# Optimization experiments

Hardware: AMD Instinct MI355X
Metric: run time of the kernel (lower is better)

## Reference

```python
import jax, jax.numpy as jnp
import numpy as np

C0, C1, ED, H, L, K = 128, 32, 64, 4, 2, 16
RADIUS = 16.0
EPS = 1e-6


def _ln(x, g, b):
    m = jnp.mean(x, -1, keepdims=True)
    v = jnp.var(x, -1, keepdims=True)
    return (x - m) * jax.lax.rsqrt(v + 1e-5) * g + b


def _gather_nodes(x, idx):
    # x [B,N,...], idx [B,N,K] -> [B,N,K,...]
    return jax.vmap(lambda xb, ib: xb[ib])(x, idx)


def _gather_pairs(e, idx):
    # e [B,N,N,ED], idx [B,N,K] -> [B,N,K,ED]  (batched_index_select on dim=2)
    return jax.vmap(lambda eb, ib: jnp.take_along_axis(eb, ib[..., None], axis=1))(e, idx)


def _fiber_norm(f0, f1, g0, b0, g1, b1):
    # deg-0: LayerNorm + gelu; deg-1: phase-preserving norm on channel magnitudes
    f0n = jax.nn.gelu(_ln(f0, g0, b0))
    n1 = jnp.linalg.norm(f1, axis=-1)                       # [B,N,C1]
    f1n = f1 / (n1 + EPS)[..., None] * jax.nn.gelu(_ln(n1, g1, b1))[..., None]
    return f0n, f1n


def _tfn_kv(f0j, f1j, y1, r, WA, WB):
    # Equivariant TFN edge kernel: paths 0->0(l=0), 1->0(l=1), 0->1(l=1),
    # 1->1(l=0), 1->1(l=1, cross), 1->1(l=2, traceless Y2) with radial gates r.
    r1, r2, r3, r4, r5, r6 = jnp.split(
        r, [C0, C0 + C1, 2 * C0 + C1, 2 * C0 + 2 * C1, 2 * C0 + 3 * C1], axis=-1)
    dot1 = jnp.einsum('bnkcm,bnkm->bnkc', f1j, y1)          # [B,N,K,C1]
    in0 = jnp.concatenate([r1 * f0j, r2 * dot1], -1)        # [B,N,K,C0+C1]
    k0 = jnp.einsum('oc,bnkc->bnko', WA, in0)               # [B,N,K,C0]
    p3 = (r3 * f0j)[..., None] * y1[..., None, :]           # [B,N,K,C0,3]
    p4 = r4[..., None] * f1j
    p5 = r5[..., None] * jnp.cross(f1j, y1[..., None, :])
    p6 = r6[..., None] * (y1[..., None, :] * dot1[..., None] - f1j / 3.0)
    in1 = jnp.concatenate([p3, p4, p5, p6], axis=-2)        # [B,N,K,C0+3*C1,3]
    k1 = jnp.einsum('oc,bnkcm->bnkom', WB, in1)             # [B,N,K,C1,3]
    return k0, k1


def reference(node_feats, pair_feats, coords, eln_g, eln_b, Wi0, Wi1,
              ln0_g, ln0_b, n1_g, n1_b, Wq0, Wq1, WrK, WrV, WkA, WkB, WvA, WvB,
              Wb, Wo0, Wo1, alpha_attn, lnf0_g, lnf0_b, nf1_g, nf1_b,
              Wf0a, Wf0b, Wf1a, Wf1b, alpha_ff, Wp0, Wp1):
    B, N = node_feats.shape[:2]
    Na, CA, Cc, Oo = [coords[..., i, :] for i in range(4)]          # each [B,N,3]
    f1_in = jnp.stack([Na, Cc, Oo], axis=-2) - CA[..., None, :]     # [B,N,3,3]
    # kNN graph on CA coords (exclude self), radius mask at 16A
    d2 = jnp.sum((CA[:, :, None] - CA[:, None, :]) ** 2, -1)        # [B,N,N]
    d2 = d2 + jnp.eye(N, dtype=d2.dtype) * 1e9
    nv, idx = jax.lax.top_k(-d2, K)                                 # idx [B,N,K]
    dist = jnp.sqrt(jnp.maximum(-nv, 0.0))
    mask = dist <= RADIUS
    rel_pos = _gather_nodes(CA, idx) - CA[:, :, None]               # [B,N,K,3]
    rel_b = jax.lax.stop_gradient(rel_pos)                          # basis on detached rel_pos
    y1 = rel_b / (jnp.linalg.norm(rel_b, axis=-1, keepdims=True) + EPS)
    edges = _ln(_gather_pairs(pair_feats, idx), eln_g, eln_b)       # [B,N,K,ED]
    # project in
    f0 = jnp.einsum('oc,bnc->bno', Wi0, node_feats)                 # [B,N,C0]
    f1 = jnp.einsum('oc,bncm->bnom', Wi1, f1_in)                    # [B,N,C1,3]
    dh0, dh1 = C0 // H, C1 // H
    scale = 1.0 / np.sqrt(dh0 + 3 * dh1)
    for l in range(L):
        # ---- attention block (prenorm -> TFN attention -> rezero residual)
        x0, x1 = _fiber_norm(f0, f1, ln0_g[l], ln0_b[l], n1_g[l], n1_b[l])
        q0 = jnp.einsum('oc,bnc->bno', Wq0[l], x0)
        q1 = jnp.einsum('oc,bncm->bnom', Wq1[l], x1)
        x0j = _gather_nodes(x0, idx)                                # [B,N,K,C0]
        x1j = _gather_nodes(x1, idx)                                # [B,N,K,C1,3]
        rk = jnp.einsum('re,bnke->bnkr', WrK[l], edges)
        rv = jnp.einsum('re,bnke->bnkr', WrV[l], edges)
        k0, k1 = _tfn_kv(x0j, x1j, y1, rk, WkA[l], WkB[l])
        v0, v1 = _tfn_kv(x0j, x1j, y1, rv, WvA[l], WvB[l])
        q0h = q0.reshape(B, N, H, dh0)
        q1h = q1.reshape(B, N, H, dh1, 3)
        k0h = k0.reshape(B, N, K, H, dh0)
        k1h = k1.reshape(B, N, K, H, dh1, 3)
        v0h = v0.reshape(B, N, K, H, dh0)
        v1h = v1.reshape(B, N, K, H, dh1, 3)
        logits = (jnp.einsum('bnhc,bnkhc->bnhk', q0h, k0h)
                  + jnp.einsum('bnhcm,bnkhcm->bnhk', q1h, k1h)) * scale
        logits = logits + jnp.einsum('he,bnke->bnhk', Wb[l], edges)
        logits = jnp.where(mask[:, :, None, :], logits, -1e9)
        attn = jax.nn.softmax(logits, axis=-1)
        o0 = jnp.einsum('bnhk,bnkhc->bnhc', attn, v0h).reshape(B, N, C0)
        o1 = jnp.einsum('bnhk,bnkhcm->bnhcm', attn, v1h).reshape(B, N, C1, 3)
        f0 = f0 + alpha_attn[l] * jnp.einsum('oc,bnc->bno', Wo0[l], o0)
        f1 = f1 + alpha_attn[l] * jnp.einsum('oc,bncm->bnom', Wo1[l], o1)
        # ---- fiber feedforward (prenorm -> FF -> rezero residual)
        x0, x1 = _fiber_norm(f0, f1, lnf0_g[l], lnf0_b[l], nf1_g[l], nf1_b[l])
        h0 = jnp.einsum('oh,bnh->bno', Wf0b[l],
                        jax.nn.gelu(jnp.einsum('hc,bnc->bnh', Wf0a[l], x0)))
        h1 = jnp.einsum('hc,bncm->bnhm', Wf1a[l], x1)
        nh = jnp.linalg.norm(h1, axis=-1)
        h1 = h1 * (jax.nn.gelu(nh) / (nh + EPS))[..., None]
        h1 = jnp.einsum('oh,bnhm->bnom', Wf1b[l], h1)
        f0 = f0 + alpha_ff[l] * h0
        f1 = f1 + alpha_ff[l] * h1
    # project out + _to_output
    node_out = jnp.einsum('oc,bnc->bno', Wp0, f0)                   # [B,N,128]
    coords_out = CA[:, :, None, :] + jnp.einsum('oc,bncm->bnom', Wp1, f1)  # [B,N,3,3]
    return node_out, coords_out


def setup_inputs() -> dict:
    key = jax.random.key(0)
    ks = iter(jax.random.split(key, 64))
    def rn(shape, scale=1.0):
        return (jax.random.normal(next(ks), shape) * scale).astype(jnp.float32)
    B, N = 1, 1024
    RC = 2 * C0 + 4 * C1
    ca = jnp.cumsum(rn((B, N, 3), 1.5), axis=1)          # protein-like chain
    coords = ca[:, :, None, :] + rn((B, N, 4, 3), 0.5)
    inp = dict(
        node_feats=rn((B, N, 128)),
        pair_feats=rn((B, N, N, ED)),
        coords=coords,
        eln_g=jnp.ones((ED,), jnp.float32), eln_b=jnp.zeros((ED,), jnp.float32),
        Wi0=rn((C0, 128), 128 ** -0.5), Wi1=rn((C1, 3), 3 ** -0.5),
        ln0_g=jnp.ones((L, C0), jnp.float32), ln0_b=jnp.zeros((L, C0), jnp.float32),
        n1_g=jnp.ones((L, C1), jnp.float32), n1_b=jnp.zeros((L, C1), jnp.float32),
        Wq0=rn((L, C0, C0), C0 ** -0.5), Wq1=rn((L, C1, C1), C1 ** -0.5),
        WrK=rn((L, RC, ED), ED ** -0.5), WrV=rn((L, RC, ED), ED ** -0.5),
        WkA=rn((L, C0, C0 + C1), (C0 + C1) ** -0.5),
        WkB=rn((L, C1, C0 + 3 * C1), (C0 + 3 * C1) ** -0.5),
        WvA=rn((L, C0, C0 + C1), (C0 + C1) ** -0.5),
        WvB=rn((L, C1, C0 + 3 * C1), (C0 + 3 * C1) ** -0.5),
        Wb=rn((L, H, ED), ED ** -0.5),
        Wo0=rn((L, C0, C0), C0 ** -0.5), Wo1=rn((L, C1, C1), C1 ** -0.5),
        alpha_attn=jnp.full((L,), 0.5, jnp.float32),
        lnf0_g=jnp.ones((L, C0), jnp.float32), lnf0_b=jnp.zeros((L, C0), jnp.float32),
        nf1_g=jnp.ones((L, C1), jnp.float32), nf1_b=jnp.zeros((L, C1), jnp.float32),
        Wf0a=rn((L, 4 * C0, C0), C0 ** -0.5), Wf0b=rn((L, C0, 4 * C0), (4 * C0) ** -0.5),
        Wf1a=rn((L, 4 * C1, C1), C1 ** -0.5), Wf1b=rn((L, C1, 4 * C1), (4 * C1) ** -0.5),
        alpha_ff=jnp.full((L,), 0.5, jnp.float32),
        Wp0=rn((128, C0), C0 ** -0.5), Wp1=rn((3, C1), C1 ** -0.5),
    )
    return inp
```

## Files before the change

### kernel.cpp

```cpp
#include <hip/hip_runtime.h>
#include <hip/hip_bf16.h>
#include <math.h>

static constexpr int NN  = 1024;
static constexpr int KK  = 16;
static constexpr int C0c = 128;
static constexpr int C1c = 32;
static constexpr int EDc = 64;
static constexpr int Lc  = 2;
static constexpr int ENUM = NN * KK;
static constexpr int PL   = NN * C1c;
static constexpr int X1HS = NN * 32;
#define SCALE_ATTN 0.13363062095621219f

typedef __attribute__((ext_vector_type(8))) short s8v;
typedef __attribute__((ext_vector_type(4))) float f4v;

__device__ __forceinline__ float wsum64(float v) {
    for (int o = 32; o > 0; o >>= 1) v += __shfl_xor(v, o);
    return v;
}
__device__ __forceinline__ float gsum16(float v) {
    for (int o = 8; o > 0; o >>= 1) v += __shfl_xor(v, o, 16);
    return v;
// ... 52 lines not shown
        const int wid = tid >> 6, lane = tid & 63;
        const int n = (bx - cvb) * 4 + wid;
        const float cx = ca[n * 3 + 0], cy = ca[n * 3 + 1], cz = ca[n * 3 + 2];
        float d[16];
#pragma unroll
        for (int s = 0; s < 16; ++s) {
            int i = s * 64 + lane;
            float dx = cx - ca[i * 3 + 0], dy = cy - ca[i * 3 + 1], dz = cz - ca[i * 3 + 2];
            float d2 = dx * dx + dy * dy + dz * dz;
            d[s] = (i == n) ? 1e9f : d2;
        }
        for (int t = 0; t < KK; ++t) {
            float best = 1e30f; int bi = 0;
#pragma unroll
            for (int s = 0; s < 16; ++s) {
                int i = s * 64 + lane;
                float v = d[s];
                if (v < best || (v == best && i < bi)) { best = v; bi = i; }
            }
#pragma unroll
            for (int o = 32; o > 0; o >>= 1) {
                float ov = __shfl_xor(best, o);
                int   oi = __shfl_xor(bi, o);
                if (ov < best || (ov == best && oi < bi)) { best = ov; bi = oi; }
            }
            const int j = bi;
            if (lane == 0) {
                idx[n * KK + t] = j;
                float dist = sqrtf(best);
                maskf[n * KK + t] = (dist <= 16.0f) ? 1.0f : 0.0f;
                float rx = ca[j * 3 + 0] - cx, ry = ca[j * 3 + 1] - cy, rz = ca[j * 3 + 2] - cz;
                float nrm = sqrtf(rx * rx + ry * ry + rz * rz) + 1e-6f;
                y1[(n * KK + t) * 3 + 0] = rx / nrm;
                y1[(n * KK + t) * 3 + 1] = ry / nrm;
                y1[(n * KK + t) * 3 + 2] = rz / nrm;
            }
            const int js = j >> 6, jl = j & 63;
#pragma unroll
            for (int s = 0; s < 16; ++s)
                if (s == js && jl == lane) d[s] = 2e30f;
        }
        return;
    }
    int g = (bx - cvb - 256) * 256 + tid;
    if (g >= NN * 32) return;
    int n = g >> 5, c = g & 31;
    float w0 = Wi1[c * 3 + 0], w1 = Wi1[c * 3 + 1], w2 = Wi1[c * 3 + 2];
#pragma unroll
    for (int m = 0; m < 3; ++m) {
        float cav = coords[(n * 4 + 1) * 3 + m];
        float a0 = coords[(n * 4 + 0) * 3 + m] - cav;
        float a1 = coords[(n * 4 + 2) * 3 + m] - cav;
        float a2 = coords[(n * 4 + 3) * 3 + m] - cav;
        f1p[m * PL + n * 32 + c] = w0 * a0 + w1 * a1 + w2 * a2;
    }
}

__global__ __launch_bounds__(256) void edge_f0_kernel(const float* __restrict__ pair,
                                                      const int* __restrict__ idx,
                                                      const float* __restrict__ g,
                                                      const float* __restrict__ b,
                                                      const float* __restrict__ Wb,
                                                      unsigned short* __restrict__ edges_h,
                                                      float* __restrict__ biasb,
                                                      const unsigned short* __restrict__ nf_h,
                                                      const unsigned short* __restrict__ Wi0_h,
                                                      float* __restrict__ f0) {
    const int t = threadIdx.x, wid = t >> 6, lane = t & 63;
    if (blockIdx.x < ENUM / 4) {
        const int e = blockIdx.x * 4 + wid;
        const int n = e >> 4;
        const int j = idx[e];
        float v = pair[((size_t)n * NN + j) * EDc + lane];
        float m = wsum64(v) * (1.0f / 64.0f);
        float d = v - m;
        float var = wsum64(d * d) * (1.0f / 64.0f);
        float nv = d * rsqrtf(var + 1e-5f) * g[lane] + b[lane];
        edges_h[e * EDc + lane] = f2bf(nv);
#pragma unroll
        for (int l = 0; l < 2; ++l)
#pragma unroll
            for (int h = 0; h < 4; ++h) {
                float tt = wsum64(nv * Wb[(l * 4 + h) * 64 + lane]);
                if (lane == 0) biasb[(size_t)l * ENUM * 4 + e * 4 + h] = tt;
            }
        return;
    }
    int rel = blockIdx.x - ENUM / 4;
    const int mt = rel & 7, ntc = rel >> 3;
    const int m0 = mt * 128 + wid * 32, n0 = ntc * 32;
    const int c16 = lane & 15, g8 = (lane >> 4) * 8, g4 = (lane >> 4) * 4;
    f4v acc[2][2];
#pragma unroll
    for (int a = 0; a < 2; ++a)
#pragma unroll
        for (int bq = 0; bq < 2; ++bq) acc[a][bq] = f4v{0.f, 0.f, 0.f, 0.f};
    const unsigned short* Ap = nf_h + (size_t)(m0 + c16) * 128 + g8;
    const unsigned short* Bp = Wi0_h + (size_t)(n0 + c16) * 128 + g8;
#pragma unroll
    for (int kc = 0; kc < 128; kc += 32) {
        s8v a0 = ld8(Ap + kc);
        s8v a1 = ld8(Ap + 16 * 128 + kc);
        s8v b0 = ld8(Bp + kc);
        s8v b1 = ld8(Bp + 16 * 128 + kc);
        acc[0][0] = mfma16(a0, b0, acc[0][0]);
        acc[0][1] = mfma16(a0, b1, acc[0][1]);
        acc[1][0] = mfma16(a1, b0, acc[1][0]);
        acc[1][1] = mfma16(a1, b1, acc[1][1]);
    }
#pragma unroll
    for (int fm = 0; fm < 2; ++fm)
#pragma unroll
        for (int r = 0; r < 4; ++r) {
            const int m = m0 + fm * 16 + g4 + r;
#pragma unroll
            for (int fn = 0; fn < 2; ++fn)
                f0[(size_t)m * 128 + n0 + fn * 16 + c16] = acc[fm][fn][r];
        }
}

__global__ __launch_bounds__(256) void fnorm1_kernel(const float* __restrict__ f0,
                                                     const float* __restrict__ f1p,
                                                     const float* __restrict__ g0,
                                                     const float* __restrict__ b0,
                                                     const float* __restrict__ g1,
                                                     const float* __restrict__ b1,
                                                     unsigned short* __restrict__ x0h,
                                                     unsigned short* __restrict__ x1h) {
    const int wid = threadIdx.x >> 6, lane = threadIdx.x & 63;
    const int n = blockIdx.x * 4 + wid;
    float va = f0[n * 128 + lane], vb = f0[n * 128 + lane + 64];
    float m = wsum64(va + vb) * (1.0f / 128.0f);
    float da = va - m, db = vb - m;
    float var = wsum64(da * da + db * db) * (1.0f / 128.0f);
    float rs = rsqrtf(var + 1e-5f);
    x0h[n * 128 + lane]      = f2bf(gelu_f(da * rs * g0[lane] + b0[lane]));
    x0h[n * 128 + lane + 64] = f2bf(gelu_f(db * rs * g0[lane + 64] + b0[lane + 64]));
    int c = lane & 31;
    float h0 = f1p[0 * PL + n * 32 + c];
    float h1 = f1p[1 * PL + n * 32 + c];
    float h2 = f1p[2 * PL + n * 32 + c];
    float n1 = sqrtf(h0 * h0 + h1 * h1 + h2 * h2);
    float ms = wsum64(n1) * (1.0f / 64.0f);
    float dd = n1 - ms;
    float vv = wsum64(dd * dd) * (1.0f / 64.0f);
    float sc = gelu_f(dd * rsqrtf(vv + 1e-5f) * g1[c] + b1[c]) / (n1 + 1e-6f);
    if (lane < 32) {
        x1h[0 * X1HS + n * 32 + c] = f2bf(h0 * sc);
        x1h[1 * X1HS + n * 32 + c] = f2bf(h1 * sc);
        x1h[2 * X1HS + n * 32 + c] = f2bf(h2 * sc);
    }
}

static constexpr int EKV_LDS = (64 * 168 + 64 * 136 + 3 * 64 * 104) * 2;

__global__ __launch_bounds__(256) void edge_kv_kernel(
    const unsigned short* __restrict__ edges_h,
    const unsigned short* __restrict__ WrK, const unsigned short* __restrict__ WrV,
    const unsigned short* __restrict__ WkA, const unsigned short* __restrict__ WvA,
    const unsigned short* __restrict__ WkB, const unsigned short* __restrict__ WvB,
    const unsigned short* __restrict__ x0h, const unsigned short* __restrict__ x1h,
    const int* __restrict__ idx, const float* __restrict__ y1,
    unsigned short* __restrict__ k0h, unsigned short* __restrict__ v0h,
    unsigned short* __restrict__ uKh, unsigned short* __restrict__ uVh,
    unsigned short* __restrict__ k1ph, unsigned short* __restrict__ v1ph,
    const unsigned short* __restrict__ Wq0l, const unsigned short* __restrict__ Wq1l,
    float* __restrict__ q0, float* __restrict__ q1p) {
    extern __shared__ unsigned short lsm[];
    const int t = threadIdx.x, w = t >> 6, l = t & 63;
    const int c16 = l & 15, g8 = (l >> 4) * 8, g4 = (l >> 4) * 4;
    const int bid = blockIdx.x;
    if (bid < 512) {
        unsigned short* in0L = lsm;
        unsigned short* inUL = lsm + 64 * 168;
        unsigned short* inWL = lsm + 64 * 168 + 64 * 136;
        const int s = bid >> 8, et = bid & 255, e0 = et * 64;
        const unsigned short* Wr = s ? WrV : WrK;
        const unsigned short* WA = s ? WvA : WkA;
        const unsigned short* WB = s ? WvB : WkB;
        unsigned short* K0o = s ? v0h : k0h;
        unsigned short* Uo  = s ? uVh : uKh;
        unsigned short* K1o = s ? v1ph : k1ph;
#pragma unroll 1
        for (int ti = w; ti < 24; ti += 4) {
            const int esub = ti & 1, rt = ti >> 1;
            const int e0w = e0 + esub * 32, r0 = rt * 32;
            f4v acc[2][2];
#pragma unroll
            for (int a = 0; a < 2; ++a)
#pragma unroll
                for (int bq = 0; bq < 2; ++bq) acc[a][bq] = f4v{0.f, 0.f, 0.f, 0.f};
#pragma unroll
            for (int kc = 0; kc < 64; kc += 32) {
                s8v a0 = ld8(edges_h + (size_t)(e0w + c16) * 64 + kc + g8);
                s8v a1 = ld8(edges_h + (size_t)(e0w + 16 + c16) * 64 + kc + g8);
                s8v b0 = ld8(Wr + (size_t)(r0 + c16) * 64 + kc + g8);
                s8v b1 = ld8(Wr + (size_t)(r0 + 16 + c16) * 64 + kc + g8);
                acc[0][0] = mfma16(a0, b0, acc[0][0]);
                acc[0][1] = mfma16(a0, b1, acc[0][1]);
                acc[1][0] = mfma16(a1, b0, acc[1][0]);
                acc[1][1] = mfma16(a1, b1, acc[1][1]);
            }
#pragma unroll
            for (int fm = 0; fm < 2; ++fm)
#pragma unroll
                for (int r = 0; r < 4; ++r) {
                    const int el = esub * 32 + fm * 16 + g4 + r;
                    const int e = e0 + el;
                    const int j = idx[e];
                    float ya = y1[e * 3 + 0], yb = y1[e * 3 + 1], yc = y1[e * 3 + 2];
#pragma unroll
                    for (int fn = 0; fn < 2; ++fn) {
                        const float av = acc[fm][fn][r];
                        const int col = r0 + fn * 16 + c16;
                        if (r0 < 128) {
                            in0L[el * 168 + col] = f2bf(av * bf2f(x0h[j * 128 + col]));
                        } else if (r0 < 160) {
                            int c = col - 128;
                            float d1 = bf2f(x1h[0 * X1HS + j * 32 + c]) * ya
                                     + bf2f(x1h[1 * X1HS + j * 32 + c]) * yb
                                     + bf2f(x1h[2 * X1HS + j * 32 + c]) * yc;
                            in0L[el * 168 + col] = f2bf(av * d1);
                        } else if (r0 < 288) {
                            int c = col - 160;
                            inUL[el * 136 + c] = f2bf(av * bf2f(x0h[j * 128 + c]));
                        } else {
                            int c = (r0 < 320) ? (col - 288) : (r0 < 352) ? (col - 320) : (col - 352);
                            float fx = bf2f(x1h[0 * X1HS + j * 32 + c]);
                            float fy = bf2f(x1h[1 * X1HS + j * 32 + c]);
                            float fz = bf2f(x1h[2 * X1HS + j * 32 + c]);
                            float w0, w1, w2; int off;
                            if (r0 < 320) {
                                off = 0; w0 = av * fx; w1 = av * fy; w2 = av * fz;
                            } else if (r0 < 352) {
                                off = 32;
                                w0 = av * (fy * yc - fz * yb);
                                w1 = av * (fz * ya - fx * yc);
                                w2 = av * (fx * yb - fy * ya);
                            } else {
                                off = 64;
                                float d1 = fx * ya + fy * yb + fz * yc;
                                w0 = av * (ya * d1 - fx * (1.0f / 3.0f));
                                w1 = av * (yb * d1 - fy * (1.0f / 3.0f));
                                w2 = av * (yc * d1 - fz * (1.0f / 3.0f));
                            }
                            inWL[0 * 64 * 104 + el * 104 + off + c] = f2bf(w0);
                            inWL[1 * 64 * 104 + el * 104 + off + c] = f2bf(w1);
                            inWL[2 * 64 * 104 + el * 104 + off + c] = f2bf(w2);
                        }
                    }
                }
        }
        __syncthreads();
#pragma unroll 1
        for (int ti = w; ti < 16; ti += 4) {
            const unsigned short* Ab; const unsigned short* Bb;
            unsigned short* Cb;
            int apit, K, ldb, ldcq, esub;
            if (ti < 8) {
                esub = ti & 1; int nt = ti >> 1;
                Ab = in0L; apit = 168; K = 160;
                Bb = WA + (size_t)(nt * 32) * 160; ldb = 160;
                Cb = K0o + (size_t)(e0 + esub * 32) * 128 + nt * 32; ldcq = 128;
            } else if (ti < 10) {
                esub = ti - 8;
                Ab = inUL; apit = 136; K = 128; Bb = WB; ldb = 224;
                Cb = Uo + (size_t)(e0 + esub * 32) * 32; ldcq = 32;
            } else {
                int id = ti - 10; int m = id >> 1; esub = id & 1;
                Ab = inWL + m * 64 * 104; apit = 104; K = 96;
                Bb = WB + 128; ldb = 224;
                Cb = K1o + ((size_t)m * ENUM + e0 + esub * 32) * 32; ldcq = 32;
            }
            const int m0l = esub * 32;
            f4v acc[2][2];
#pragma unroll
            for (int a = 0; a < 2; ++a)
#pragma unroll
                for (int bq = 0; bq < 2; ++bq) acc[a][bq] = f4v{0.f, 0.f, 0.f, 0.f};
            for (int kc = 0; kc < K; kc += 32) {
                s8v a0 = *(const s8v*)&Ab[(m0l + c16) * apit + kc + g8];
                s8v a1 = *(const s8v*)&Ab[(m0l + 16 + c16) * apit + kc + g8];
                s8v b0 = ld8(Bb + (size_t)c16 * ldb + kc + g8);
                s8v b1 = ld8(Bb + (size_t)(16 + c16) * ldb + kc + g8);
                acc[0][0] = mfma16(a0, b0, acc[0][0]);
                acc[0][1] = mfma16(a0, b1, acc[0][1]);
                acc[1][0] = mfma16(a1, b0, acc[1][0]);
                acc[1][1] = mfma16(a1, b1, acc[1][1]);
            }
#pragma unroll
            for (int fm = 0; fm < 2; ++fm)
#pragma unroll
                for (int r = 0; r < 4; ++r) {
                    const int lr = fm * 16 + g4 + r;
#pragma unroll
                    for (int fn = 0; fn < 2; ++fn)
                        Cb[(size_t)lr * ldcq + fn * 16 + c16] = f2bf(acc[fm][fn][r]);
                }
        }
        return;
    }
    const int rel = bid - 512;
    const unsigned short* A; const unsigned short* B;
    float* C; int K, lda2, ldb2, ldc2, m0, n0;
    if (rel < 32) {
        int mt = rel & 7, nt = rel >> 3;
        A = x0h; B = Wq0l; C = q0;
        K = 128; lda2 = 128; ldb2 = 128; ldc2 = 128;
        m0 = mt * 128 + w * 32; n0 = nt * 32;
    } else {
        int k = rel - 32; int pl = k >> 3; int mt = k & 7;
        A = x1h + (size_t)pl * X1HS; B = Wq1l; C = q1p + (size_t)pl * PL;
        K = 32; lda2 = 32; ldb2 = 32; ldc2 = 32;
        m0 = mt * 128 + w * 32; n0 = 0;
    }
    f4v acc[2][2];
#pragma unroll
    for (int a = 0; a < 2; ++a)
#pragma unroll
        for (int bq = 0; bq < 2; ++bq) acc[a][bq] = f4v{0.f, 0.f, 0.f, 0.f};
    const unsigned short* Ap = A + (size_t)(m0 + c16) * lda2 + g8;
    const unsigned short* Bp = B + (size_t)(n0 + c16) * ldb2 + g8;
    for (int kc = 0; kc < K; kc += 32) {
        s8v a0 = ld8(Ap + kc);
        s8v a1 = ld8(Ap + 16 * lda2 + kc);
        s8v b0 = ld8(Bp + kc);
        s8v b1 = ld8(Bp + 16 * ldb2 + kc);
        acc[0][0] = mfma16(a0, b0, acc[0][0]);
        acc[0][1] = mfma16(a0, b1, acc[0][1]);
        acc[1][0] = mfma16(a1, b0, acc[1][0]);
        acc[1][1] = mfma16(a1, b1, acc[1][1]);
    }
#pragma unroll
    for (int fm = 0; fm < 2; ++fm)
#pragma unroll
        for (int r = 0; r < 4; ++r) {
            const int m = m0 + fm * 16 + g4 + r;
#pragma unroll
            for (int fn = 0; fn < 2; ++fn)
                C[(size_t)m * ldc2 + n0 + fn * 16 + c16] = acc[fm][fn][r];
        }
}

__global__ __launch_bounds__(256) void attn_core(const float* __restrict__ q0,
                                                 const float* __restrict__ q1p,
                                                 const unsigned short* __restrict__ k0h,
                                                 const unsigned short* __restrict__ k1ph,
                                                 const unsigned short* __restrict__ v0h,
                                                 const unsigned short* __restrict__ v1ph,
                                                 const unsigned short* __restrict__ uKh,
                                                 const unsigned short* __restrict__ uVh,
                                                 const float* __restrict__ biasb,
                                                 const float* __restrict__ maskf,
                                                 const float* __restrict__ y1,
                                                 unsigned short* __restrict__ o0h,
                                                 unsigned short* __restrict__ o1h) {
    __shared__ float q0s[4][128];
    __shared__ float q1s[4][96];
    __shared__ float attns[4][64];
    const int wid = threadIdx.x >> 6, lane = threadIdx.x & 63;
    const int n = blockIdx.x * 4 + wid;
    q0s[wid][lane]      = q0[n * 128 + lane];
    q0s[wid][lane + 64] = q0[n * 128 + lane + 64];
    if (lane < 32) {
#pragma unroll
        for (int m = 0; m < 3; ++m) q1s[wid][m * 32 + lane] = q1p[m * PL + n * 32 + lane];
    }
    __syncthreads();
    {
        const int h = lane >> 4, k = lane & 15;
        const int e = n * KK + k;
        float acc = 0.f;
        const unsigned short* kr = k0h + (size_t)e * 128 + h * 32;
#pragma unroll
        for (int c8 = 0; c8 < 4; ++c8) {
            s8v kv = ld8(kr + c8 * 8);
#pragma unroll
            for (int j = 0; j < 8; ++j)
                acc += q0s[wid][h * 32 + c8 * 8 + j] * bf2f((unsigned short)kv[j]);
        }
        s8v uv = ld8(uKh + (size_t)e * 32 + h * 8);
#pragma unroll
        for (int m = 0; m < 3; ++m) {
            float yv = y1[e * 3 + m];
            s8v k1v = ld8(k1ph + ((size_t)m * ENUM + e) * 32 + h * 8);
#pragma unroll
            for (int c = 0; c < 8; ++c)
                acc += q1s[wid][m * 32 + h * 8 + c] *
                       (bf2f((unsigned short)k1v[c]) + bf2f((unsigned short)uv[c]) * yv);
        }
        acc = acc * SCALE_ATTN + biasb[e * 4 + h];
        if (maskf[e] == 0.0f) acc = -1e9f;
        float mx = gmax16(acc);
        float ex = expf(acc - mx);
        float sm = gsum16(ex);
        attns[wid][lane] = ex / sm;
    }
    __syncthreads();
    const int g = lane & 15, kq = lane >> 4;
    {
        float o[8] = {};
        const float* aw = &attns[wid][(g >> 2) * 16];
#pragma unroll
        for (int kk2 = 0; kk2 < 4; ++kk2) {
            int kk = kq * 4 + kk2;
            float a = aw[kk];
            s8v v = ld8(v0h + (size_t)(n * KK + kk) * 128 + g * 8);
#pragma unroll
            for (int j = 0; j < 8; ++j) o[j] += a * bf2f((unsigned short)v[j]);
        }
#pragma unroll
        for (int j = 0; j < 8; ++j) {
            o[j] += __shfl_xor(o[j], 16);
            o[j] += __shfl_xor(o[j], 32);
        }
        if (kq == 0) {
            s8v r;
#pragma unroll
            for (int j = 0; j < 8; ++j) r[j] = (short)f2bf(o[j]);
            *(s8v*)&o0h[(size_t)n * 128 + g * 8] = r;
        }
    }
    {
        float o[8] = {};
        const int plane = g >> 2, cg = g & 3;
        if (g < 12) {
            const float* aw = &attns[wid][cg * 16];
#pragma unroll
            for (int kk2 = 0; kk2 < 4; ++kk2) {
                int kk = kq * 4 + kk2;
                int e2 = n * KK + kk;
                float a = aw[kk];
                float yv = y1[e2 * 3 + plane];
                s8v v = ld8(v1ph + ((size_t)plane * ENUM + e2) * 32 + cg * 8);
                s8v u = ld8(uVh + (size_t)e2 * 32 + cg * 8);
#pragma unroll
                for (int j = 0; j < 8; ++j)
                    o[j] += a * (bf2f((unsigned short)v[j]) + bf2f((unsigned short)u[j]) * yv);
            }
        }
#pragma unroll
        for (int j = 0; j < 8; ++j) {
            o[j] += __shfl_xor(o[j], 16);
            o[j] += __shfl_xor(o[j], 32);
        }
        if (kq == 0 && g < 12) {
            s8v r;
#pragma unroll
            for (int j = 0; j < 8; ++j) r[j] = (short)f2bf(o[j]);
            *(s8v*)&o1h[((size_t)plane * NN + n) * 32 + cg * 8] = r;
        }
    }
}

template <int MODE>
__global__ __launch_bounds__(512) void fused_post(
    const unsigned short* __restrict__ o0h, const unsigned short* __restrict__ o1h,
    float* __restrict__ f0, float* __restrict__ f1p,
    const unsigned short* __restrict__ Wo0h, const unsigned short* __restrict__ Wo1h,
    const unsigned short* __restrict__ Wf0ah, const unsigned short* __restrict__ Wf0bh,
    const unsigned short* __restrict__ Wf1ah, const unsigned short* __restrict__ Wf1bh,
    const float* __restrict__ alA, const float* __restrict__ alF,
    const float* __restrict__ lnf0_g, const float* __restrict__ lnf0_b,
    const float* __restrict__ nf1_g, const float* __restrict__ nf1_b,
    const float* __restrict__ ln0n_g, const float* __restrict__ ln0n_b,
    const float* __restrict__ n1n_g, const float* __restrict__ n1n_b,
    unsigned short* __restrict__ x0h, unsigned short* __restrict__ x1h,
    const unsigned short* __restrict__ Wp0h, const float* __restrict__ Wp1,
    const float* __restrict__ coords, float* __restrict__ out) {
    __shared__ float f0s[16][132];
    __shared__ float f1s[3][16][36];
    __shared__ unsigned short x0s[16][136];
    __shared__ float x1s[3][16][36];
    __shared__ unsigned short hs[16][520];
    __shared__ unsigned short h1b[3][16][136];
    const int t = threadIdx.x, w = t >> 6, l = t & 63;
    const int c16 = l & 15, g8 = (l >> 4) * 8, g4 = (l >> 4) * 4;
    const int n0 = blockIdx.x * 16;
    const float aA = alA[0], aF = alF[0];

// ... 151 lines not shown
            }
            float s = gsum16(n1v[0] + n1v[1]);
            float mn = s * (1.0f / 32.0f);
            float d0 = n1v[0] - mn, d1 = n1v[1] - mn;
            float vv = gsum16(d0 * d0 + d1 * d1);
            float rs = rsqrtf(vv * (1.0f / 32.0f) + 1e-5f);
#pragma unroll
            for (int q = 0; q < 2; ++q) {
                int c = sub + q * 16;
                float sc = gelu_f((n1v[q] - mn) * rs * n1n_g[c] + n1n_b[c]) / (n1v[q] + 1e-6f);
                x1h[(size_t)0 * X1HS + (n0 + node) * 32 + c] = f2bf(p[q][0] * sc);
                x1h[(size_t)1 * X1HS + (n0 + node) * 32 + c] = f2bf(p[q][1] * sc);
                x1h[(size_t)2 * X1HS + (n0 + node) * 32 + c] = f2bf(p[q][2] * sc);
            }
        }
    } else {
#pragma unroll
        for (int it = 0; it < 4; ++it) {
            int g = t + it * 512;
            int row = g >> 7, col = g & 127;
            x0s[row][col] = f2bf(f0s[row][col]);
        }
        __syncthreads();
        f4v acc = f4v{0.f, 0.f, 0.f, 0.f};
#pragma unroll
        for (int kc = 0; kc < 128; kc += 32) {
            s8v a = *(const s8v*)&x0s[c16][kc + g8];
            s8v b = ld8(Wp0h + (size_t)(w * 16 + c16) * 128 + g8 + kc);
            acc = mfma16(a, b, acc);
        }
        int colg = w * 16 + c16;
#pragma unroll
        for (int r = 0; r < 4; ++r)
            out[(size_t)(n0 + g4 + r) * 128 + colg] = acc[r];
        if (t < 144) {
            int node = t / 9, rr = t % 9, o = rr / 3, m = rr % 3;
            float a = coords[((size_t)(n0 + node) * 4 + 1) * 3 + m];
            for (int c = 0; c < 32; ++c) a += Wp1[o * 32 + c] * f1s[m][node][c];
            out[NN * 128 + ((size_t)(n0 + node) * 3 + o) * 3 + m] = a;
        }
    }
}

extern "C" void kernel_launch(void* const* d_in, const int* in_sizes, int n_in,
                              void* d_out, int out_size, void* d_ws, size_t ws_size,
                              hipStream_t stream) {
    (void)in_sizes; (void)n_in; (void)out_size; (void)ws_size;
    const float* node_feats = (const float*)d_in[0];
    const float* pair       = (const float*)d_in[1];
    const float* coords     = (const float*)d_in[2];
    const float* eln_g      = (const float*)d_in[3];
    const float* eln_b      = (const float*)d_in[4];
    const float* Wi0        = (const float*)d_in[5];
    const float* Wi1        = (const float*)d_in[6];
    const float* ln0_g      = (const float*)d_in[7];
    const float* ln0_b      = (const float*)d_in[8];
    const float* n1_g       = (const float*)d_in[9];
    const float* n1_b       = (const float*)d_in[10];
    const float* Wq0        = (const float*)d_in[11];
    const float* Wq1        = (const float*)d_in[12];
    const float* WrK        = (const float*)d_in[13];
    const float* WrV        = (const float*)d_in[14];
    const float* WkA        = (const float*)d_in[15];
    const float* WkB        = (const float*)d_in[16];
    const float* WvA        = (const float*)d_in[17];
    const float* WvB        = (const float*)d_in[18];
    const float* Wb         = (const float*)d_in[19];
    const float* Wo0        = (const float*)d_in[20];
    const float* Wo1        = (const float*)d_in[21];
    const float* alpha_attn = (const float*)d_in[22];
    const float* lnf0_g     = (const float*)d_in[23];
    const float* lnf0_b     = (const float*)d_in[24];
    const float* nf1_g      = (const float*)d_in[25];
    const float* nf1_b      = (const float*)d_in[26];
    const float* Wf0a       = (const float*)d_in[27];
    const float* Wf0b       = (const float*)d_in[28];
    const float* Wf1a       = (const float*)d_in[29];
    const float* Wf1b       = (const float*)d_in[30];
    const float* alpha_ff   = (const float*)d_in[31];
    const float* Wp0        = (const float*)d_in[32];
    const float* Wp1        = (const float*)d_in[33];
    float* out = (float*)d_out;

    float* ws = (float*)d_ws;
    size_t off = 0;
    int*   idx   = (int*)(ws + off); off += NN * KK;
    float* maskf = ws + off;         off += NN * KK;
    float* y1    = ws + off;         off += NN * KK * 3;
    float* f0    = ws + off;         off += NN * C0c;
    float* f1p   = ws + off;         off += 3 * PL;
    float* q0    = ws + off;         off += NN * C0c;
    float* q1p   = ws + off;         off += 3 * PL;
    float* biasb = ws + off;         off += (size_t)2 * ENUM * 4;
    off = (off + 3) & ~(size_t)3;
    unsigned short* up = (unsigned short*)(ws + off);
    size_t uo = 0;
    unsigned short* edges_h = up + uo; uo += (size_t)ENUM * 64;
    unsigned short* x0h     = up + uo; uo += (size_t)NN * 128;
    unsigned short* x1h     = up + uo; uo += (size_t)3 * X1HS;
    unsigned short* nf_h    = up + uo; uo += (size_t)NN * 128;
    unsigned short* k0h     = up + uo; uo += (size_t)ENUM * 128;
    unsigned short* v0h     = up + uo; uo += (size_t)ENUM * 128;
    unsigned short* uKh     = up + uo; uo += (size_t)ENUM * 32;
    unsigned short* uVh     = up + uo; uo += (size_t)ENUM * 32;
    unsigned short* k1ph    = up + uo; uo += (size_t)3 * ENUM * 32;
    unsigned short* v1ph    = up + uo; uo += (size_t)3 * ENUM * 32;
    unsigned short* o0h     = up + uo; uo += (size_t)NN * 128;
    unsigned short* o1h     = up + uo; uo += (size_t)3 * NN * 32;
    unsigned short* WrK_h   = up + uo; uo += 2 * 24576;
    unsigned short* WrV_h   = up + uo; uo += 2 * 24576;
    unsigned short* WkA_h   = up + uo; uo += 2 * 20480;
    unsigned short* WvA_h   = up + uo; uo += 2 * 20480;
    unsigned short* WkB_h   = up + uo; uo += 2 * 7168;
    unsigned short* WvB_h   = up + uo; uo += 2 * 7168;
    unsigned short* Wq0_h   = up + uo; uo += 2 * 16384;
    unsigned short* Wq1_h   = up + uo; uo += 2 * 1024;
    unsigned short* Wo0_h   = up + uo; uo += 2 * 16384;
    unsigned short* Wo1_h   = up + uo; uo += 2 * 1024;
    unsigned short* Wf0a_h  = up + uo; uo += 2 * 65536;
    unsigned short* Wf0b_h  = up + uo; uo += 2 * 65536;
    unsigned short* Wf1a_h  = up + uo; uo += 2 * 4096;
    unsigned short* Wf1b_h  = up + uo; uo += 2 * 4096;
    unsigned short* Wp0_h   = up + uo; uo += 16384;
    unsigned short* Wi0_h   = up + uo; uo += 16384;

    CvJobs cj; cj.n = 17;
    cj.j[0]  = {WrK,  WrK_h,  2 * 24576};
    cj.j[1]  = {WrV,  WrV_h,  2 * 24576};
    cj.j[2]  = {WkA,  WkA_h,  2 * 20480};
    cj.j[3]  = {WvA,  WvA_h,  2 * 20480};
    cj.j[4]  = {WkB,  WkB_h,  2 * 7168};
    cj.j[5]  = {WvB,  WvB_h,  2 * 7168};
    cj.j[6]  = {Wq0,  Wq0_h,  2 * 16384};
    cj.j[7]  = {Wq1,  Wq1_h,  2 * 1024};
    cj.j[8]  = {Wo0,  Wo0_h,  2 * 16384};
    cj.j[9]  = {Wo1,  Wo1_h,  2 * 1024};
    cj.j[10] = {Wf0a, Wf0a_h, 2 * 65536};
    cj.j[11] = {Wf0b, Wf0b_h, 2 * 65536};
    cj.j[12] = {Wf1a, Wf1a_h, 2 * 4096};
    cj.j[13] = {Wf1b, Wf1b_h, 2 * 4096};
    cj.j[14] = {Wp0,  Wp0_h,  16384};
    cj.j[15] = {Wi0,  Wi0_h,  16384};
    cj.j[16] = {node_feats, nf_h, NN * 128};
    cj.total = 2*24576*2 + 2*20480*2 + 2*7168*2 + 2*16384 + 2*1024 + 2*16384
             + 2*1024 + 2*65536*2 + 2*4096*2 + 16384 + 16384 + NN*128;
    const int cvb = (cj.total + 255) / 256;

    setup_kernel<<<cvb + 256 + 128, 256, 0, stream>>>(cj, cvb, coords, idx, maskf, y1, Wi1, f1p);
    edge_f0_kernel<<<ENUM / 4 + 32, 256, 0, stream>>>(pair, idx, eln_g, eln_b, Wb,
                                                      edges_h, biasb, nf_h, Wi0_h, f0);
    fnorm1_kernel<<<NN / 4, 256, 0, stream>>>(f0, f1p, ln0_g, ln0_b, n1_g, n1_b, x0h, x1h);

    for (int l = 0; l < Lc; ++l) {
        edge_kv_kernel<<<568, 256, EKV_LDS, stream>>>(
            edges_h,
            WrK_h + (size_t)l * 24576, WrV_h + (size_t)l * 24576,
            WkA_h + (size_t)l * 20480, WvA_h + (size_t)l * 20480,
            WkB_h + (size_t)l * 7168,  WvB_h + (size_t)l * 7168,
            x0h, x1h, idx, y1,
            k0h, v0h, uKh, uVh, k1ph, v1ph,
            Wq0_h + (size_t)l * 16384, Wq1_h + (size_t)l * 1024, q0, q1p);
        attn_core<<<NN / 4, 256, 0, stream>>>(q0, q1p, k0h, k1ph, v0h, v1ph, uKh, uVh,
            biasb + (size_t)l * ENUM * 4, maskf, y1, o0h, o1h);
        if (l == 0) {
            fused_post<0><<<NN / 16, 512, 0, stream>>>(
                o0h, o1h, f0, f1p,
                Wo0_h, Wo1_h, Wf0a_h, Wf0b_h, Wf1a_h, Wf1b_h,
                alpha_attn + 0, alpha_ff + 0,
                lnf0_g, lnf0_b, nf1_g, nf1_b,
                ln0_g + 128, ln0_b + 128, n1_g + 32, n1_b + 32,
                x0h, x1h, nullptr, nullptr, nullptr, nullptr);
        } else {
            fused_post<1><<<NN / 16, 512, 0, stream>>>(
                o0h, o1h, f0, f1p,
                Wo0_h + 16384, Wo1_h + 1024, Wf0a_h + 65536, Wf0b_h + 65536,
                Wf1a_h + 4096, Wf1b_h + 4096,
                alpha_attn + 1, alpha_ff + 1,
                lnf0_g + 128, lnf0_b + 128, nf1_g + 32, nf1_b + 32,
                nullptr, nullptr, nullptr, nullptr,
                nullptr, nullptr, Wp0_h, Wp1, coords, out);
        }
    }
}
```

Baseline: 242.6 us.

## Stage gathered neighbor features in LDS and process K and V in one block

The edge K/V kernel now uses 512-thread blocks that each handle 64 edges for both the K and V passes. Each block first gathers the neighbor x0/x1 rows and y1 vectors into shared memory, so the epilogue reads those instead of scattered global loads. Each gather is done once per block instead of twice, once per K and V side. The Q projection blocks are remapped to one 32x32 tile per warp to fit the new launch of 284 blocks. The cost is more LDS per block and an extra sync per pass, which may lower occupancy.

Result: faster. 229.7 us (-5.3%).

```diff
diff --git a/kernel.cpp b/kernel.cpp
--- a/kernel.cpp
+++ b/kernel.cpp
@@ -228,9 +228,15 @@
     }
 }
 
-static constexpr int EKV_LDS = (64 * 168 + 64 * 136 + 3 * 64 * 104) * 2;
-
-__global__ __launch_bounds__(256) void edge_kv_kernel(
+static constexpr int LS_IN0 = 0;
+static constexpr int LS_INU = 64 * 168;
+static constexpr int LS_INW = LS_INU + 64 * 136;
+static constexpr int LS_X0  = LS_INW + 3 * 64 * 104;
+static constexpr int LS_X1  = LS_X0 + 64 * 128;
+static constexpr int LS_Y   = LS_X1 + 3 * 64 * 32;
+static constexpr int EKV_LDS2 = LS_Y * 2 + 64 * 3 * 4;
+
+__global__ __launch_bounds__(512) void edge_kv2(
     const unsigned short* __restrict__ edges_h,
     const unsigned short* __restrict__ WrK, const unsigned short* __restrict__ WrV,
     const unsigned short* __restrict__ WkA, const unsigned short* __restrict__ WvA,
@@ -246,149 +252,169 @@
     const int t = threadIdx.x, w = t >> 6, l = t & 63;
     const int c16 = l & 15, g8 = (l >> 4) * 8, g4 = (l >> 4) * 4;
     const int bid = blockIdx.x;
-    if (bid < 512) {
-        unsigned short* in0L = lsm;
-        unsigned short* inUL = lsm + 64 * 168;
-        unsigned short* inWL = lsm + 64 * 168 + 64 * 136;
-        const int s = bid >> 8, et = bid & 255, e0 = et * 64;
-        const unsigned short* Wr = s ? WrV : WrK;
-        const unsigned short* WA = s ? WvA : WkA;
-        const unsigned short* WB = s ? WvB : WkB;
-        unsigned short* K0o = s ? v0h : k0h;
-        unsigned short* Uo  = s ? uVh : uKh;
-        unsigned short* K1o = s ? v1ph : k1ph;
+    if (bid < 256) {
+        unsigned short* in0L = lsm + LS_IN0;
+        unsigned short* inUL = lsm + LS_INU;
+        unsigned short* inWL = lsm + LS_INW;
+        unsigned short* x0L  = lsm + LS_X0;
+        unsigned short* x1L  = lsm + LS_X1;
+        float* yL = (float*)(lsm + LS_Y);
+        const int e0 = bid * 64;
+        for (int c = t; c < 1024; c += 512) {
+            int row = c >> 4, sub = c & 15;
+            int j = idx[e0 + row];
+            *(s8v*)&x0L[row * 128 + sub * 8] = ld8(x0h + (size_t)j * 128 + sub * 8);
+        }
+        for (int c = t; c < 768; c += 512) {
+            int plane = c >> 8, rem = c & 255;
+            int row = rem >> 2, sub = rem & 3;
+            int j = idx[e0 + row];
+            *(s8v*)&x1L[(plane * 64 + row) * 32 + sub * 8] =
+                ld8(x1h + (size_t)plane * X1HS + (size_t)j * 32 + sub * 8);
+        }
+        if (t < 192) yL[t] = y1[e0 * 3 + t];
+        __syncthreads();
 #pragma unroll 1
-        for (int ti = w; ti < 24; ti += 4) {
-            const int esub = ti & 1, rt = ti >> 1;
-            const int e0w = e0 + esub * 32, r0 = rt * 32;
-            f4v acc[2][2];
-#pragma unroll
-            for (int a = 0; a < 2; ++a)
-#pragma unroll
-                for (int bq = 0; bq < 2; ++bq) acc[a][bq] = f4v{0.f, 0.f, 0.f, 0.f};
-#pragma unroll
-            for (int kc = 0; kc < 64; kc += 32) {
-                s8v a0 = ld8(edges_h + (size_t)(e0w + c16) * 64 + kc + g8);
-                s8v a1 = ld8(edges_h + (size_t)(e0w + 16 + c16) * 64 + kc + g8);
-                s8v b0 = ld8(Wr + (size_t)(r0 + c16) * 64 + kc + g8);
-                s8v b1 = ld8(Wr + (size_t)(r0 + 16 + c16) * 64 + kc + g8);
-                acc[0][0] = mfma16(a0, b0, acc[0][0]);
-                acc[0][1] = mfma16(a0, b1, acc[0][1]);
-                acc[1][0] = mfma16(a1, b0, acc[1][0]);
-                acc[1][1] = mfma16(a1, b1, acc[1][1]);
-            }
-#pragma unroll
-            for (int fm = 0; fm < 2; ++fm)
-#pragma unroll
-                for (int r = 0; r < 4; ++r) {
-                    const int el = esub * 32 + fm * 16 + g4 + r;
-                    const int e = e0 + el;
-                    const int j = idx[e];
-                    float ya = y1[e * 3 + 0], yb = y1[e * 3 + 1], yc = y1[e * 3 + 2];
-#pragma unroll
-                    for (int fn = 0; fn < 2; ++fn) {
-                        const float av = acc[fm][fn][r];
-                        const int col = r0 + fn * 16 + c16;
-                        if (r0 < 128) {
-                            in0L[el * 168 + col] = f2bf(av * bf2f(x0h[j * 128 + col]));
-                        } else if (r0 < 160) {
-                            int c = col - 128;
-                            float d1 = bf2f(x1h[0 * X1HS + j * 32 + c]) * ya
-                                     + bf2f(x1h[1 * X1HS + j * 32 + c]) * yb
-                                     + bf2f(x1h[2 * X1HS + j * 32 + c]) * yc;
-                            in0L[el * 168 + col] = f2bf(av * d1);
-                        } else if (r0 < 288) {
-                            int c = col - 160;
-                            inUL[el * 136 + c] = f2bf(av * bf2f(x0h[j * 128 + c]));
-                        } else {
-                            int c = (r0 < 320) ? (col - 288) : (r0 < 352) ? (col - 320) : (col - 352);
-                            float fx = bf2f(x1h[0 * X1HS + j * 32 + c]);
-                            float fy = bf2f(x1h[1 * X1HS + j * 32 + c]);
-                            float fz = bf2f(x1h[2 * X1HS + j * 32 + c]);
-                            float w0, w1, w2; int off;
-                            if (r0 < 320) {
-                                off = 0; w0 = av * fx; w1 = av * fy; w2 = av * fz;
-                            } else if (r0 < 352) {
-                                off = 32;
-                                w0 = av * (fy * yc - fz * yb);
-                                w1 = av * (fz * ya - fx * yc);
-                                w2 = av * (fx * yb - fy * ya);
+        for (int s = 0; s < 2; ++s) {
+            const unsigned short* Wr = s ? WrV : WrK;
+            const unsigned short* WA = s ? WvA : WkA;
+            const unsigned short* WB = s ? WvB : WkB;
+            unsigned short* K0o = s ? v0h : k0h;
+            unsigned short* Uo  = s ? uVh : uKh;
+            unsigned short* K1o = s ? v1ph : k1ph;
+#pragma unroll 1
+            for (int ti = w; ti < 24; ti += 8) {
+                const int esub = ti & 1, rt = ti >> 1;
+                const int e0w = e0 + esub * 32, r0 = rt * 32;
+                f4v acc[2][2];
+#pragma unroll
+                for (int a = 0; a < 2; ++a)
+#pragma unroll
+                    for (int bq = 0; bq < 2; ++bq) acc[a][bq] = f4v{0.f, 0.f, 0.f, 0.f};
+#pragma unroll
+                for (int kc = 0; kc < 64; kc += 32) {
+                    s8v a0 = ld8(edges_h + (size_t)(e0w + c16) * 64 + kc + g8);
+                    s8v a1 = ld8(edges_h + (size_t)(e0w + 16 + c16) * 64 + kc + g8);
+                    s8v b0 = ld8(Wr + (size_t)(r0 + c16) * 64 + kc + g8);
+                    s8v b1 = ld8(Wr + (size_t)(r0 + 16 + c16) * 64 + kc + g8);
+                    acc[0][0] = mfma16(a0, b0, acc[0][0]);
+                    acc[0][1] = mfma16(a0, b1, acc[0][1]);
+                    acc[1][0] = mfma16(a1, b0, acc[1][0]);
+                    acc[1][1] = mfma16(a1, b1, acc[1][1]);
+                }
+#pragma unroll
+                for (int fm = 0; fm < 2; ++fm)
+#pragma unroll
+                    for (int r = 0; r < 4; ++r) {
+                        const int el = esub * 32 + fm * 16 + g4 + r;
+                        float ya = yL[el * 3 + 0], yb = yL[el * 3 + 1], yc = yL[el * 3 + 2];
+#pragma unroll
+                        for (int fn = 0; fn < 2; ++fn) {
+                            const float av = acc[fm][fn][r];
+                            const int col = r0 + fn * 16 + c16;
+                            if (r0 < 128) {
+                                in0L[el * 168 + col] = f2bf(av * bf2f(x0L[el * 128 + col]));
+                            } else if (r0 < 160) {
+                                int c = col - 128;
+                                float d1 = bf2f(x1L[(0 * 64 + el) * 32 + c]) * ya
+                                         + bf2f(x1L[(1 * 64 + el) * 32 + c]) * yb
+                                         + bf2f(x1L[(2 * 64 + el) * 32 + c]) * yc;
+                                in0L[el * 168 + col] = f2bf(av * d1);
+                            } else if (r0 < 288) {
+                                int c = col - 160;
+                                inUL[el * 136 + c] = f2bf(av * bf2f(x0L[el * 128 + c]));
                             } else {
-                                off = 64;
-                                float d1 = fx * ya + fy * yb + fz * yc;
-                                w0 = av * (ya * d1 - fx * (1.0f / 3.0f));
-                                w1 = av * (yb * d1 - fy * (1.0f / 3.0f));
-                                w2 = av * (yc * d1 - fz * (1.0f / 3.0f));
+                                int c = (r0 < 320) ? (col - 288) : (r0 < 352) ? (col - 320) : (col - 352);
+                                float fx = bf2f(x1L[(0 * 64 + el) * 32 + c]);
+                                float fy = bf2f(x1L[(1 * 64 + el) * 32 + c]);
+                                float fz = bf2f(x1L[(2 * 64 + el) * 32 + c]);
+                                float w0, w1, w2; int off;
+                                if (r0 < 320) {
+                                    off = 0; w0 = av * fx; w1 = av * fy; w2 = av * fz;
+                                } else if (r0 < 352) {
+                                    off = 32;
+                                    w0 = av * (fy * yc - fz * yb);
+                                    w1 = av * (fz * ya - fx * yc);
+                                    w2 = av * (fx * yb - fy * ya);
+                                } else {
+                                    off = 64;
+                                    float d1 = fx * ya + fy * yb + fz * yc;
+                                    w0 = av * (ya * d1 - fx * (1.0f / 3.0f));
+                                    w1 = av * (yb * d1 - fy * (1.0f / 3.0f));
+                                    w2 = av * (yc * d1 - fz * (1.0f / 3.0f));
+                                }
+                                inWL[0 * 64 * 104 + el * 104 + off + c] = f2bf(w0);
+                                inWL[1 * 64 * 104 + el * 104 + off + c] = f2bf(w1);
+                                inWL[2 * 64 * 104 + el * 104 + off + c] = f2bf(w2);
                             }
-                            inWL[0 * 64 * 104 + el * 104 + off + c] = f2bf(w0);
-                            inWL[1 * 64 * 104 + el * 104 + off + c] = f2bf(w1);
-                            inWL[2 * 64 * 104 + el * 104 + off + c] = f2bf(w2);
                         }
                     }
+            }
+            __syncthreads();
+#pragma unroll 1
+            for (int ti = w; ti < 16; ti += 8) {
+                const unsigned short* Ab; const unsigned short* Bb;
+                unsigned short* Cb;
+                int apit, K, ldb, ldcq, esub;
+                if (ti < 8) {
+                    esub = ti & 1; int nt = ti >> 1;
+                    Ab = in0L; apit = 168; K = 160;
+                    Bb = WA + (size_t)(nt * 32) * 160; ldb = 160;
+                    Cb = K0o + (size_t)(e0 + esub * 32) * 128 + nt * 32; ldcq = 128;
+                } else if (ti < 10) {
+                    esub = ti - 8;
+                    Ab = inUL; apit = 136; K = 128; Bb = WB; ldb = 224;
+                    Cb = Uo + (size_t)(e0 + esub * 32) * 32; ldcq = 32;
+                } else {
+                    int id = ti - 10; int m = id >> 1; esub = id & 1;
+                    Ab = inWL + m * 64 * 104; apit = 104; K = 96;
+                    Bb = WB + 128; ldb = 224;
+                    Cb = K1o + ((size_t)m * ENUM + e0 + esub * 32) * 32; ldcq = 32;
                 }
-        }
-        __syncthreads();
-#pragma unroll 1
-        for (int ti = w; ti < 16; ti += 4) {
-            const unsigned short* Ab; const unsigned short* Bb;
-            unsigned short* Cb;
-            int apit, K, ldb, ldcq, esub;
-            if (ti < 8) {
-                esub = ti & 1; int nt = ti >> 1;
-                Ab = in0L; apit = 168; K = 160;
-                Bb = WA + (size_t)(nt * 32) * 160; ldb = 160;
-                Cb = K0o + (size_t)(e0 + esub * 32) * 128 + nt * 32; ldcq = 128;
-            } else if (ti < 10) {
-                esub = ti - 8;
-                Ab = inUL; apit = 136; K = 128; Bb = WB; ldb = 224;
-                Cb = Uo + (size_t)(e0 + esub * 32) * 32; ldcq = 32;
-            } else {
-                int id = ti - 10; int m = id >> 1; esub = id & 1;
-                Ab = inWL + m * 64 * 104; apit = 104; K = 96;
-                Bb = WB + 128; ldb = 224;
-                Cb = K1o + ((size_t)m * ENUM + e0 + esub * 32) * 32; ldcq = 32;
+                const int m0l = esub * 32;
+                f4v acc[2][2];
+#pragma unroll
+                for (int a = 0; a < 2; ++a)
+#pragma unroll
+                    for (int bq = 0; bq < 2; ++bq) acc[a][bq] = f4v{0.f, 0.f, 0.f, 0.f};
+                for (int kc = 0; kc < K; kc += 32) {
+                    s8v a0 = *(const s8v*)&Ab[(m0l + c16) * apit + kc + g8];
+                    s8v a1 = *(const s8v*)&Ab[(m0l + 16 + c16) * apit + kc + g8];
+                    s8v b0 = ld8(Bb + (size_t)c16 * ldb + kc + g8);
+                    s8v b1 = ld8(Bb + (size_t)(16 + c16) * ldb + kc + g8);
+                    acc[0][0] = mfma16(a0, b0, acc[0][0]);
+                    acc[0][1] = mfma16(a0, b1, acc[0][1]);
+                    acc[1][0] = mfma16(a1, b0, acc[1][0]);
+                    acc[1][1] = mfma16(a1, b1, acc[1][1]);
+                }
+#pragma unroll
+                for (int fm = 0; fm < 2; ++fm)
+#pragma unroll
+                    for (int r = 0; r < 4; ++r) {
+                        const int lr = fm * 16 + g4 + r;
+#pragma unroll
+                        for (int fn = 0; fn < 2; ++fn)
+                            Cb[(size_t)lr * ldcq + fn * 16 + c16] = f2bf(acc[fm][fn][r]);
+                    }
             }
-            const int m0l = esub * 32;
-            f4v acc[2][2];
-#pragma unroll
-            for (int a = 0; a < 2; ++a)
-#pragma unroll
-                for (int bq = 0; bq < 2; ++bq) acc[a][bq] = f4v{0.f, 0.f, 0.f, 0.f};
-            for (int kc = 0; kc < K; kc += 32) {
-                s8v a0 = *(const s8v*)&Ab[(m0l + c16) * apit + kc + g8];
-                s8v a1 = *(const s8v*)&Ab[(m0l + 16 + c16) * apit + kc + g8];
-                s8v b0 = ld8(Bb + (size_t)c16 * ldb + kc + g8);
-                s8v b1 = ld8(Bb + (size_t)(16 + c16) * ldb + kc + g8);
-                acc[0][0] = mfma16(a0, b0, acc[0][0]);
-                acc[0][1] = mfma16(a0, b1, acc[0][1]);
-                acc[1][0] = mfma16(a1, b0, acc[1][0]);
-                acc[1][1] = mfma16(a1, b1, acc[1][1]);
-            }
-#pragma unroll
-            for (int fm = 0; fm < 2; ++fm)
-#pragma unroll
-                for (int r = 0; r < 4; ++r) {
-                    const int lr = fm * 16 + g4 + r;
-#pragma unroll
-                    for (int fn = 0; fn < 2; ++fn)
-                        Cb[(size_t)lr * ldcq + fn * 16 + c16] = f2bf(acc[fm][fn][r]);
-                }
+            __syncthreads();
         }
         return;
     }
-    const int rel = bid - 512;
+    const int wt = (bid - 256) * 8 + w;
     const unsigned short* A; const unsigned short* B;
-    float* C; int K, lda2, ldb2, ldc2, m0, n0;
-    if (rel < 32) {
-        int mt = rel & 7, nt = rel >> 3;
+    float* C; int K, lda2, m0, n0, ldc2;
+    if (wt < 128) {
+        int rowt = wt >> 2, colt = wt & 3;
         A = x0h; B = Wq0l; C = q0;
-        K = 128; lda2 = 128; ldb2 = 128; ldc2 = 128;
-        m0 = mt * 128 + w * 32; n0 = nt * 32;
+        K = 128; lda2 = 128; ldc2 = 128;
+        m0 = rowt * 32; n0 = colt * 32;
     } else {
-        int k = rel - 32; int pl = k >> 3; int mt = k & 7;
+        int k = wt - 128;
+        int pl = k >> 5, rowt = k & 31;
         A = x1h + (size_t)pl * X1HS; B = Wq1l; C = q1p + (size_t)pl * PL;
-        K = 32; lda2 = 32; ldb2 = 32; ldc2 = 32;
-        m0 = mt * 128 + w * 32; n0 = 0;
+        K = 32; lda2 = 32; ldc2 = 32;
+        m0 = rowt * 32; n0 = 0;
     }
     f4v acc[2][2];
 #pragma unroll
@@ -396,12 +422,12 @@
 #pragma unroll
         for (int bq = 0; bq < 2; ++bq) acc[a][bq] = f4v{0.f, 0.f, 0.f, 0.f};
     const unsigned short* Ap = A + (size_t)(m0 + c16) * lda2 + g8;
-    const unsigned short* Bp = B + (size_t)(n0 + c16) * ldb2 + g8;
+    const unsigned short* Bp = B + (size_t)(n0 + c16) * lda2 + g8;
     for (int kc = 0; kc < K; kc += 32) {
         s8v a0 = ld8(Ap + kc);
         s8v a1 = ld8(Ap + 16 * lda2 + kc);
         s8v b0 = ld8(Bp + kc);
-        s8v b1 = ld8(Bp + 16 * ldb2 + kc);
+        s8v b1 = ld8(Bp + 16 * lda2 + kc);
         acc[0][0] = mfma16(a0, b0, acc[0][0]);
         acc[0][1] = mfma16(a0, b1, acc[0][1]);
         acc[1][0] = mfma16(a1, b0, acc[1][0]);
@@ -859,7 +885,7 @@
     fnorm1_kernel<<<NN / 4, 256, 0, stream>>>(f0, f1p, ln0_g, ln0_b, n1_g, n1_b, x0h, x1h);
 
     for (int l = 0; l < Lc; ++l) {
-        edge_kv_kernel<<<568, 256, EKV_LDS, stream>>>(
+        edge_kv2<<<284, 512, EKV_LDS2, stream>>>(
             edges_h,
             WrK_h + (size_t)l * 24576, WrV_h + (size_t)l * 24576,
             WkA_h + (size_t)l * 20480, WvA_h + (size_t)l * 20480,
```
